# Kernel optimization log

Hardware: AMD Instinct MI355X
Metric: run time of the kernel (lower is better)

Reference implementation:

```python
import jax, jax.numpy as jnp
import numpy as np

EPS = 1e-5

def layer_norm(x, g, b):
    mu = jnp.mean(x, axis=-1, keepdims=True)
    var = jnp.mean(jnp.square(x - mu), axis=-1, keepdims=True)
    return (x - mu) * jax.lax.rsqrt(var + EPS) * g + b

def setup_inputs() -> dict:
    key = jax.random.key(0)
    ks = jax.random.split(key, 12)
    I, H, N = 512, 512, 65536
    s = 0.02
    return {
        "x": jax.random.normal(ks[0], (I,), dtype=jnp.float32),
        "hiddens": jax.random.normal(ks[1], (N, H), dtype=jnp.float32),
        "Wz": jax.random.normal(ks[2], (H, I + H), dtype=jnp.float32) * s,
        "Wri": jax.random.normal(ks[3], (H, I), dtype=jnp.float32) * s,
        "Wrh": jax.random.normal(ks[4], (H, H), dtype=jnp.float32) * s,
        "Wu": jax.random.normal(ks[5], (H, I + H), dtype=jnp.float32) * s,
        "gz": jnp.ones((H,), jnp.float32), "bz": jnp.zeros((H,), jnp.float32),
        "gr": jnp.ones((H,), jnp.float32), "br": jnp.zeros((H,), jnp.float32),
        "gu": jnp.ones((H,), jnp.float32), "bu": jnp.zeros((H,), jnp.float32),
    }

def reference(x, hiddens, Wz, Wri, Wrh, Wu, gz, bz, gr, br, gu, bu):
    # hiddens: [N, H] stacked child hidden states; x: [I]
    hidden_sum = hiddens.sum(0)  # [H]
    # r gate: per-child linear + LayerNorm + sigmoid -> [N, H]
    r_pre = x @ Wri.T + hiddens @ Wrh.T  # broadcast input term over children
    r = jax.nn.sigmoid(layer_norm(r_pre, gr, br))
    # z gate over (input, sum of child hiddens)
    z = jax.nn.sigmoid(layer_norm(jnp.concatenate([x, hidden_sum]) @ Wz.T, gz, bz))
    # candidate with reset-gated child sum
    u = jnp.tanh(layer_norm(jnp.concatenate([x, (r * hiddens).sum(0)]) @ Wu.T, gu, bu))
    h = z * hidden_sum + (1.0 - z) * u
    return h
```

## Files before the change

kernel.cpp:

```cpp
#include <hip/hip_runtime.h>

#define HDIM 512
#define BM 64

typedef __attribute__((ext_vector_type(8))) short bf16x8;
typedef __attribute__((ext_vector_type(4))) float f32x4;

__device__ __forceinline__ unsigned short f2bf(float f){
  union { float f; unsigned int u; } c; c.f = f;
  unsigned int u = c.u;
  unsigned int r = u + 0x7fffu + ((u >> 16) & 1u);
  return (unsigned short)(r >> 16);
}
__device__ __forceinline__ float bf2f(unsigned short b){
  union { unsigned int u; float f; } c; c.u = ((unsigned int)b) << 16;
  return c.f;
}
__device__ __forceinline__ unsigned int pack_trunc(float a, float b){
  return __builtin_amdgcn_perm(__float_as_uint(b), __float_as_uint(a), 0x07060302u);
}

__global__ __launch_bounds__(256) void prep_k(const float* __restrict__ Wrh,
    unsigned short* __restrict__ wpack, const float* __restrict__ Wri,
    const float* __restrict__ x, float* __restrict__ xwri)
{
  int b = blockIdx.x;
  if (b < 128){
    int t    = b * 256 + threadIdx.x;
    int lane = t & 63;
    int g    = t >> 6;
    int ni   = g & 3;
    int kkk  = (g >> 2) & 15;
    int wc   = g >> 6;
    int row  = wc * 64 + ni * 16 + (lane & 15);
    int k0   = kkk * 32 + (lane >> 4) * 8;
    const float* src = Wrh + (size_t)row * HDIM + k0;
    float4 f0 = *(const float4*)(src);
    float4 f1 = *(const float4*)(src + 4);
    bf16x8 v;
    v[0]=(short)f2bf(f0.x); v[1]=(short)f2bf(f0.y); v[2]=(short)f2bf(f0.z); v[3]=(short)f2bf(f0.w);
    v[4]=(short)f2bf(f1.x); v[5]=(short)f2bf(f1.y); v[6]=(short)f2bf(f1.z); v[7]=(short)f2bf(f1.w);
    *(bf16x8*)(wpack + (size_t)t * 8) = v;
  } else {
    int lane = threadIdx.x & 63, wid = threadIdx.x >> 6;
    int row = (b - 128) * 4 + wid;
    const float* Wr = Wri + (size_t)row * HDIM;
    float a = 0.f;
    #pragma unroll
    for (int k = 0; k < HDIM / 64; k++) a += x[k*64 + lane] * Wr[k*64 + lane];
    #pragma unroll
    for (int m = 1; m < 64; m <<= 1) a += __shfl_xor(a, m, 64);
    if (lane == 0) xwri[row] = a;
  }
}

__global__ __launch_bounds__(512, 4) void fused_r(
    const float* __restrict__ hiddens,
    const unsigned short* __restrict__ wpack,
    const float* __restrict__ xWri,
    const float* __restrict__ gr, const float* __restrict__ br,
    float* __restrict__ psum_rh, float* __restrict__ psum_h)
{
  __shared__ short As[BM * HDIM];
  __shared__ float redS[8 * 64];
  __shared__ float redQ[8 * 64];
  __shared__ float mu_s[64], rs_s[64];

  const int tid  = threadIdx.x;
  const int lane = tid & 63;
  const int wid  = tid >> 6;
  const int llo  = lane & 15;
  const int lhi  = lane >> 4;
  const int wcol = wid * 64;
  const int r0   = blockIdx.x * BM;

  {
    int arow = tid >> 3;
    int c0   = (tid & 7) * 8;
    const float* ap = hiddens + (size_t)(r0 + arow) * HDIM + c0;
    char* asb = (char*)As + arow * 1024;
    int sw = (arow & 7) << 4;
    #pragma unroll
    for (int i = 0; i < 8; i++){
      float4 f0 = *(const float4*)(ap + i * 64);
      float4 f1 = *(const float4*)(ap + i * 64 + 4);
      uint4 v;
      v.x = pack_trunc(f0.x, f0.y);
      v.y = pack_trunc(f0.z, f0.w);
      v.z = pack_trunc(f1.x, f1.y);
      v.w = pack_trunc(f1.z, f1.w);
      *(uint4*)(asb + ((c0 * 2 + i * 128) ^ sw)) = v;
    }
  }
  __syncthreads();

  f32x4 acc[4][4];
  #pragma unroll
  for (int i = 0; i < 4; i++)
    #pragma unroll
    for (int j = 0; j < 4; j++)
      #pragma unroll
      for (int k = 0; k < 4; k++) acc[i][j][k] = 0.f;

  const bf16x8* wp = (const bf16x8*)wpack + ((size_t)wid * 16 * 4) * 64 + lane;
  #pragma unroll 2
  for (int kb = 0; kb < 8; kb++){
    #pragma unroll
    for (int kk = 0; kk < 2; kk++){
      const bf16x8* wpi = wp + (kb * 2 + kk) * 4 * 64;
      bf16x8 af[4], bfr[4];
      #pragma unroll
      for (int ni = 0; ni < 4; ni++)
        bfr[ni] = wpi[ni * 64];
      #pragma unroll
      for (int mi = 0; mi < 4; mi++){
        int row = mi * 16 + llo;
        af[mi] = *(const bf16x8*)((char*)As + row * 1024
                   + ((kb*128 + kk*64 + lhi*16) ^ ((row & 7) << 4)));
      }
      #pragma unroll
      for (int mi = 0; mi < 4; mi++)
        #pragma unroll
        for (int ni = 0; ni < 4; ni++)
          acc[mi][ni] = __builtin_amdgcn_mfma_f32_16x16x32_bf16(af[mi], bfr[ni], acc[mi][ni], 0, 0, 0);
    }
  }

  float xw[4], g4[4], b4[4];
  #pragma unroll
  for (int ni = 0; ni < 4; ni++){
    int c = wcol + ni * 16 + llo;
    xw[ni] = xWri[c];
    g4[ni] = gr[c];
    b4[ni] = br[c];
  }
  #pragma unroll
  for (int mi = 0; mi < 4; mi++){
    #pragma unroll
    for (int rr = 0; rr < 4; rr++){
      float sv = 0.f, qv = 0.f;
      #pragma unroll
      for (int ni = 0; ni < 4; ni++){
        float v = acc[mi][ni][rr] + xw[ni];
        acc[mi][ni][rr] = v;
        sv += v; qv += v * v;
      }
      #pragma unroll
      for (int m = 1; m < 16; m <<= 1){
        sv += __shfl_xor(sv, m, 64);
        qv += __shfl_xor(qv, m, 64);
      }
      if (llo == 0){
        int row = mi * 16 + lhi * 4 + rr;
        redS[wid * 64 + row] = sv;
        redQ[wid * 64 + row] = qv;
      }
    }
  }
  __syncthreads();
  if (tid < 64){
    float S = 0.f, Q = 0.f;
    #pragma unroll
    for (int w = 0; w < 8; w++){ S += redS[w * 64 + tid]; Q += redQ[w * 64 + tid]; }
    float mu  = S * (1.f / 512.f);
    float var = Q * (1.f / 512.f) - mu * mu;
    mu_s[tid] = mu;
    rs_s[tid] = rsqrtf(var + 1e-5f);
  }
  __syncthreads();

  float prh[4] = {0.f, 0.f, 0.f, 0.f};
  float ph [4] = {0.f, 0.f, 0.f, 0.f};
  #pragma unroll
  for (int mi = 0; mi < 4; mi++){
    #pragma unroll
    for (int rr = 0; rr < 4; rr++){
      int row = mi * 16 + lhi * 4 + rr;
      float mu = mu_s[row], rs = rs_s[row];
      int sw = (row & 7) << 4;
      #pragma unroll
      for (int ni = 0; ni < 4; ni++){
        float v = (acc[mi][ni][rr] - mu) * rs * g4[ni] + b4[ni];
        float r = __builtin_amdgcn_rcpf(1.f + __expf(-v));
        int col = wcol + ni * 16 + llo;
        float h = bf2f(*(const unsigned short*)((char*)As + row * 1024 + ((col * 2) ^ sw)));
        prh[ni] += r * h;
        ph [ni] += h;
      }
    }
  }
  #pragma unroll
  for (int ni = 0; ni < 4; ni++){
    prh[ni] += __shfl_xor(prh[ni], 16, 64);
    prh[ni] += __shfl_xor(prh[ni], 32, 64);
    ph [ni] += __shfl_xor(ph [ni], 16, 64);
    ph [ni] += __shfl_xor(ph [ni], 32, 64);
  }
  if (lhi == 0){
    #pragma unroll
    for (int ni = 0; ni < 4; ni++){
      int col = wcol + ni * 16 + llo;
      psum_rh[(size_t)blockIdx.x * HDIM + col] = prh[ni];
      psum_h [(size_t)blockIdx.x * HDIM + col] = ph[ni];
    }
  }
}

__global__ __launch_bounds__(256) void reduce_psums(
    const float* __restrict__ psum_rh, const float* __restrict__ psum_h,
    const float* __restrict__ x, float* __restrict__ catz, float* __restrict__ catu,
    int nblk)
{
  __shared__ float L[8][32];
  int b = blockIdx.x, t = threadIdx.x;
  if (b < 32){
    const float* P = (b < 16) ? psum_rh : psum_h;
    int c0 = (b & 15) * 32;
    int wj = t >> 5, ci = t & 31;
    float a = 0.f;
    for (int s = wj; s < nblk; s += 8) a += P[(size_t)s * 512 + c0 + ci];
    L[wj][ci] = a;
    __syncthreads();
    if (t < 32){
      float r = 0.f;
      #pragma unroll
      for (int w = 0; w < 8; w++) r += L[w][t];
      if (b < 16) catu[512 + c0 + t] = r;
      else        catz[512 + c0 + t] = r;
    }
  } else {
    int i = ((b - 32) & 1) * 256 + t;
    if (b < 34) catz[i] = x[i];
    else        catu[i] = x[i];
  }
}

__global__ __launch_bounds__(256) void matvec_zu(
    const float* __restrict__ Wz, const float* __restrict__ Wu,
    const float* __restrict__ catz, const float* __restrict__ catu,
    float* __restrict__ zpre, float* __restrict__ upre)
{
  int b = blockIdx.x, lane = threadIdx.x & 63, wid = threadIdx.x >> 6;
  int row = (b & 127) * 4 + wid;
  const float* W = (b < 128) ? Wz : Wu;
  const float* v = (b < 128) ? catz : catu;
  float*       o = (b < 128) ? zpre : upre;
  const float* Wr = W + (size_t)row * 1024;
  float a = 0.f;
  #pragma unroll
  for (int k = 0; k < 1024 / 64; k++) a += v[k*64 + lane] * Wr[k*64 + lane];
  #pragma unroll
  for (int m = 1; m < 64; m <<= 1) a += __shfl_xor(a, m, 64);
  if (lane == 0) o[row] = a;
}

__global__ __launch_bounds__(512) void finalize_k(
    const float* __restrict__ zpre, const float* __restrict__ upre,
    const float* __restrict__ gz, const float* __restrict__ bz,
    const float* __restrict__ gu, const float* __restrict__ bu,
    const float* __restrict__ catz, float* __restrict__ out)
{
  __shared__ float R[8][4];
  int t = threadIdx.x, lane = t & 63, wid = t >> 6;
  float zp = zpre[t], up = upre[t];
  float zs = zp, zq = zp * zp, us = up, uq = up * up;
  #pragma unroll
  for (int m = 1; m < 64; m <<= 1){
    zs += __shfl_xor(zs, m, 64); zq += __shfl_xor(zq, m, 64);
    us += __shfl_xor(us, m, 64); uq += __shfl_xor(uq, m, 64);
  }
  if (lane == 0){ R[wid][0] = zs; R[wid][1] = zq; R[wid][2] = us; R[wid][3] = uq; }
  __syncthreads();
  float ZS = 0.f, ZQ = 0.f, US = 0.f, UQ = 0.f;
  #pragma unroll
  for (int w = 0; w < 8; w++){ ZS += R[w][0]; ZQ += R[w][1]; US += R[w][2]; UQ += R[w][3]; }
  float zmu = ZS / 512.f, zrs = rsqrtf(ZQ / 512.f - zmu * zmu + 1e-5f);
  float umu = US / 512.f, urs = rsqrtf(UQ / 512.f - umu * umu + 1e-5f);
  float z = 1.f / (1.f + expf(-((zp - zmu) * zrs * gz[t] + bz[t])));
  float u = tanhf((up - umu) * urs * gu[t] + bu[t]);
  float hs = catz[512 + t];
  out[t] = z * hs + (1.f - z) * u;
}

extern "C" void kernel_launch(void* const* d_in, const int* in_sizes, int n_in,
                              void* d_out, int out_size, void* d_ws, size_t ws_size,
                              hipStream_t stream)
{
  const float* x   = (const float*)d_in[0];
  const float* hid = (const float*)d_in[1];
  const float* Wz  = (const float*)d_in[2];
  const float* Wri = (const float*)d_in[3];
  const float* Wrh = (const float*)d_in[4];
  const float* Wu  = (const float*)d_in[5];
  const float* gz  = (const float*)d_in[6];
  const float* bz  = (const float*)d_in[7];
  const float* gr  = (const float*)d_in[8];
  const float* br  = (const float*)d_in[9];
  const float* gu  = (const float*)d_in[10];
  const float* bu  = (const float*)d_in[11];
  (void)n_in; (void)out_size; (void)ws_size;

  const int M    = in_sizes[1] / HDIM;
  const int nblk = M / BM;

  char* ws = (char*)d_ws;
  unsigned short* wpack = (unsigned short*)ws;
  float* xwri    = (float*)(ws + 524288);
  float* psum_rh = (float*)(ws + 526336);
  float* psum_h  = (float*)(ws + 526336 + (size_t)nblk * 2048);
  char*  p2      = ws + 526336 + (size_t)nblk * 4096;
  float* catz    = (float*)p2;
  float* catu    = (float*)(p2 + 4096);
  float* zpre    = (float*)(p2 + 8192);
  float* upre    = (float*)(p2 + 10240);
  float* out     = (float*)d_out;

  hipLaunchKernelGGL(prep_k,       dim3(256),  dim3(256), 0, stream, Wrh, wpack, Wri, x, xwri);
  hipLaunchKernelGGL(fused_r,      dim3(nblk), dim3(512), 0, stream, hid, wpack, xwri, gr, br, psum_rh, psum_h);
  hipLaunchKernelGGL(reduce_psums, dim3(36),   dim3(256), 0, stream, psum_rh, psum_h, x, catz, catu, nblk);
  hipLaunchKernelGGL(matvec_zu,    dim3(256),  dim3(256), 0, stream, Wz, Wu, catz, catu, zpre, upre);
  hipLaunchKernelGGL(finalize_k,   dim3(1),    dim3(512), 0, stream, zpre, upre, gz, bz, gu, bu, catz, out);
}
```

Measured before the change: 108.1 us.

## Stream hiddens tile into LDS per k-chunk, overlapping loads with MFMA

```diff
diff --git a/kernel.cpp b/kernel.cpp
--- a/kernel.cpp
+++ b/kernel.cpp
@@ -74,56 +74,57 @@
   const int wcol = wid * 64;
   const int r0   = blockIdx.x * BM;
 
+  const int arow = tid >> 3;
+  const int ac8  = (tid & 7) * 8;
+  const float* aslice = hiddens + (size_t)(r0 + arow) * HDIM + (tid & 7) * 4;
+  char* asb = (char*)As + arow * 1024;
+  const int sw = (arow & 7) << 4;
+
+  f32x4 acc[4][4];
+  #pragma unroll
+  for (int i = 0; i < 4; i++)
+    #pragma unroll
+    for (int j = 0; j < 4; j++)
+      #pragma unroll
+      for (int k = 0; k < 4; k++) acc[i][j][k] = 0.f;
+
+  float4 pref0 = *(const float4*)(aslice);
+  float4 pref1 = *(const float4*)(aslice + 32);
   {
-    int arow = tid >> 3;
-    int c0   = (tid & 7) * 8;
-    const float* ap = hiddens + (size_t)(r0 + arow) * HDIM + c0;
-    char* asb = (char*)As + arow * 1024;
-    int sw = (arow & 7) << 4;
-    #pragma unroll
-    for (int i = 0; i < 8; i++){
-      float4 f0 = *(const float4*)(ap + i * 64);
-      float4 f1 = *(const float4*)(ap + i * 64 + 4);
-      uint4 v;
-      v.x = pack_trunc(f0.x, f0.y);
-      v.y = pack_trunc(f0.z, f0.w);
-      v.z = pack_trunc(f1.x, f1.y);
-      v.w = pack_trunc(f1.z, f1.w);
-      *(uint4*)(asb + ((c0 * 2 + i * 128) ^ sw)) = v;
-    }
-  }
-  __syncthreads();
-
-  f32x4 acc[4][4];
-  #pragma unroll
-  for (int i = 0; i < 4; i++)
-    #pragma unroll
-    for (int j = 0; j < 4; j++)
-      #pragma unroll
-      for (int k = 0; k < 4; k++) acc[i][j][k] = 0.f;
+    uint2 w; w.x = pack_trunc(pref0.x, pref0.y); w.y = pack_trunc(pref0.z, pref0.w);
+    *(uint2*)(asb + (ac8 ^ sw)) = w;
+  }
+  asm volatile("s_waitcnt lgkmcnt(0)" ::: "memory");
+  __builtin_amdgcn_s_barrier();
 
   const bf16x8* wp = (const bf16x8*)wpack + ((size_t)wid * 16 * 4) * 64 + lane;
   #pragma unroll 2
-  for (int kb = 0; kb < 8; kb++){
-    #pragma unroll
-    for (int kk = 0; kk < 2; kk++){
-      const bf16x8* wpi = wp + (kb * 2 + kk) * 4 * 64;
-      bf16x8 af[4], bfr[4];
+  for (int kb = 0; kb < 16; kb++){
+    const bf16x8* wpi = wp + kb * 4 * 64;
+    bf16x8 bfr[4];
+    #pragma unroll
+    for (int ni = 0; ni < 4; ni++) bfr[ni] = wpi[ni * 64];
+    if ((kb & 1) == 0){ if (kb + 2 < 16) pref0 = *(const float4*)(aslice + (kb + 2) * 32); }
+    else              { if (kb + 2 < 16) pref1 = *(const float4*)(aslice + (kb + 2) * 32); }
+    bf16x8 af[4];
+    #pragma unroll
+    for (int mi = 0; mi < 4; mi++){
+      int row = mi * 16 + llo;
+      af[mi] = *(const bf16x8*)((char*)As + row * 1024
+                 + ((kb * 64 + lhi * 16) ^ ((row & 7) << 4)));
+    }
+    #pragma unroll
+    for (int mi = 0; mi < 4; mi++)
       #pragma unroll
       for (int ni = 0; ni < 4; ni++)
-        bfr[ni] = wpi[ni * 64];
-      #pragma unroll
-      for (int mi = 0; mi < 4; mi++){
-        int row = mi * 16 + llo;
-        af[mi] = *(const bf16x8*)((char*)As + row * 1024
-                   + ((kb*128 + kk*64 + lhi*16) ^ ((row & 7) << 4)));
-      }
-      #pragma unroll
-      for (int mi = 0; mi < 4; mi++)
-        #pragma unroll
-        for (int ni = 0; ni < 4; ni++)
-          acc[mi][ni] = __builtin_amdgcn_mfma_f32_16x16x32_bf16(af[mi], bfr[ni], acc[mi][ni], 0, 0, 0);
-    }
+        acc[mi][ni] = __builtin_amdgcn_mfma_f32_16x16x32_bf16(af[mi], bfr[ni], acc[mi][ni], 0, 0, 0);
+    if (kb + 1 < 16){
+      float4 p = ((kb + 1) & 1) ? pref1 : pref0;
+      uint2 w; w.x = pack_trunc(p.x, p.y); w.y = pack_trunc(p.z, p.w);
+      *(uint2*)(asb + (((kb + 1) * 64 + ac8) ^ sw)) = w;
+    }
+    asm volatile("s_waitcnt lgkmcnt(0)" ::: "memory");
+    __builtin_amdgcn_s_barrier();
   }
 
   float xw[4], g4[4], b4[4];
@@ -177,13 +178,13 @@
     for (int rr = 0; rr < 4; rr++){
       int row = mi * 16 + lhi * 4 + rr;
       float mu = mu_s[row], rs = rs_s[row];
-      int sw = (row & 7) << 4;
+      int sw2 = (row & 7) << 4;
       #pragma unroll
       for (int ni = 0; ni < 4; ni++){
         float v = (acc[mi][ni][rr] - mu) * rs * g4[ni] + b4[ni];
         float r = __builtin_amdgcn_rcpf(1.f + __expf(-v));
         int col = wcol + ni * 16 + llo;
-        float h = bf2f(*(const unsigned short*)((char*)As + row * 1024 + ((col * 2) ^ sw)));
+        float h = bf2f(*(const unsigned short*)((char*)As + row * 1024 + ((col * 2) ^ sw2)));
         prh[ni] += r * h;
         ph [ni] += h;
       }
```

Measured after the change: 105.8 us. 2.2% less time.
